# Performance work log

Hardware: AMD Instinct MI355X
Metric: run time of the kernel (lower is better)

## Reference

```python
import jax, jax.numpy as jnp
import numpy as np

WORD, D, H = 512, 64, 8  # word_size, embed_dim (per-head), n_query

def setup_inputs() -> dict:
    key = jax.random.key(0)
    ks = jax.random.split(key, 9)
    B, S = 2, 4096
    sw = 1.0 / np.sqrt(WORD)
    x  = jax.random.normal(ks[0], (B, S, WORD), dtype=jnp.float32)
    Wk = jax.random.normal(ks[1], (WORD, D), dtype=jnp.float32) * sw
    bk = jnp.zeros((D,), jnp.float32)
    Wv = jax.random.normal(ks[2], (WORD, D), dtype=jnp.float32) * sw
    bv = jnp.zeros((D,), jnp.float32)
    Wq = jax.random.normal(ks[3], (H, WORD, D), dtype=jnp.float32) * sw
    bq = jnp.zeros((H, D), jnp.float32)
    Wp = jax.random.normal(ks[4], (H * D, D), dtype=jnp.float32) * (1.0 / np.sqrt(H * D))
    bp = jnp.zeros((D,), jnp.float32)
    return {"x": x, "Wq": Wq, "bq": bq, "Wk": Wk, "bk": bk, "Wv": Wv, "bv": bv, "Wp": Wp, "bp": bp}

def reference(x, Wq, bq, Wk, bk, Wv, bv, Wp, bp):
    # shared K/V across all query heads (multi-query attention)
    K = x @ Wk + bk                                   # [b, s, d]
    V = x @ Wv + bv                                   # [b, s, d]
    Q = jnp.einsum('bsw,hwd->bhsd', x, Wq) + bq[None, :, None, :]  # [b, h, s, d]
    scale = 1.0 / jnp.sqrt(jnp.float32(D))
    scores = jnp.einsum('bhsd,btd->bhst', Q, K) * scale  # [b, h, s, t]
    attn = jax.nn.softmax(scores, axis=-1)
    Z = jnp.einsum('bhst,btd->bhsd', attn, V)            # [b, h, s, d]
    B, _, S, _ = Z.shape
    Zc = jnp.transpose(Z, (0, 2, 1, 3)).reshape(B, S, H * D)  # concat heads
    return Zc @ Wp + bp                                   # [b, s, d]
```

## Files before the change

kernel.cpp:

```cpp
#include <hip/hip_runtime.h>
#include <hip/hip_bf16.h>
#include <stdint.h>

#define BB 2
#define SS 4096
#define WW 512
#define DD 64
#define HH 8
#define QSCALE 0.1803368801111244f

typedef __hip_bfloat16 bf16;
typedef __bf16 bf16x8 __attribute__((ext_vector_type(8)));
typedef float f32x16 __attribute__((ext_vector_type(16)));
typedef unsigned int u32x4 __attribute__((ext_vector_type(4)));
typedef unsigned int u32x2 __attribute__((ext_vector_type(2)));

union U4 { u32x4 u4; unsigned int u[4]; bf16x8 v; };

__device__ __forceinline__ float ldv(const float* p, size_t i) { return p[i]; }
__device__ __forceinline__ float ldv(const bf16* p, size_t i)  { return __bfloat162float(p[i]); }

__device__ __forceinline__ unsigned short f2bu(float f) {
    union Ub { bf16 b; unsigned short u; } t;
    t.b = __float2bfloat16(f);
    return t.u;
}

__device__ __forceinline__ float fast_exp2(float x) {
#if __has_builtin(__builtin_amdgcn_exp2f)
    return __builtin_amdgcn_exp2f(x);
#else
    return exp2f(x);
#endif
}

__device__ __forceinline__ f32x16 mfma_bf16(bf16x8 a, bf16x8 b, f32x16 c) {
    return __builtin_amdgcn_mfma_f32_32x32x16_bf16(a, b, c, 0, 0, 0);
}

__device__ __forceinline__ unsigned int pk_bf16(float lo, float hi) {
    unsigned int a = __float_as_uint(lo) + 0x8000u;
    unsigned int b = __float_as_uint(hi) + 0x8000u;
    return __builtin_amdgcn_perm(b, a, 0x07060302u);
}

__device__ __forceinline__ int block_detect(const void* raw, int* cntLds)
{
    if (threadIdx.x == 0) *cntLds = 0;
    __syncthreads();
    const bf16* xb = (const bf16*)raw;
    const float v = __bfloat162float(xb[2 * threadIdx.x]);
    const float a = fabsf(v);
    const bool insane = !(v == v) || (a >= 1.0e4f) || (a != 0.0f && a <= 1.0e-8f);
    const unsigned long long m = __ballot(insane);
    if ((threadIdx.x & 63) == 0) atomicAdd(cntLds, __popcll(m));
    __syncthreads();
    return (*cntLds * 2 > 256) ? 1 : 0;
}

template<typename T> struct StReg;
template<> struct StReg<bf16>  { u32x4 v; };
template<> struct StReg<float> { float4 a, b; };

__device__ __forceinline__ void stld(StReg<bf16>& r, const bf16* p, size_t i) {
    r.v = *(const u32x4*)((const unsigned short*)p + i);
}
__device__ __forceinline__ void stld(StReg<float>& r, const float* p, size_t i) {
    r.a = *(const float4*)(p + i);
    r.b = *(const float4*)(p + i + 4);
}
__device__ __forceinline__ u32x4 stpack(const StReg<bf16>& r) { return r.v; }
__device__ __forceinline__ u32x4 stpack(const StReg<float>& r) {
    u32x4 w;
    w[0] = pk_bf16(r.a.x, r.a.y); w[1] = pk_bf16(r.a.z, r.a.w);
    w[2] = pk_bf16(r.b.x, r.b.y); w[3] = pk_bf16(r.b.z, r.b.w);
    return w;
}

template<typename T>
__device__ __forceinline__ void prep_w_body(
    const T* Wq, const T* bq, const T* Wk, const T* bk,
    const T* Wv, const T* bv, const T* Wp, const T* bp,
    unsigned short* Wb, float* bb, float (*Tt)[65], int pwblk)
{
    const int tid = threadIdx.x;
    const int cg = pwblk >> 3, wg = pwblk & 7;
    const int c0 = cg * 64, w0 = wg * 64;
    const T* src = (cg == 0) ? Wk : (cg == 1) ? Wv
                 : (cg == 10) ? Wp : (Wq + (size_t)(cg - 2) * WW * DD);
    const float scale = (cg >= 2 && cg < 10) ? QSCALE : 1.0f;

    #pragma unroll
    for (int i = 0; i < 16; ++i) {
        const int e = i * 256 + tid, w = e >> 6, d = e & 63;
        Tt[w][d] = ldv(src, (size_t)(w0 + w) * DD + d) * scale;
    }
    __syncthreads();
    #pragma unroll
    for (int i = 0; i < 16; ++i) {
        const int e = i * 256 + tid, d = e >> 6, w = e & 63;
        Wb[(size_t)(c0 + d) * WW + w0 + w] = f2bu(Tt[w][d]);
    }
    if (pwblk == 0) {
        #pragma unroll
        for (int i = 0; i < 3; ++i) {
            const int c = tid + i * 256;
            if (c < 704) {
                float v;
                if (c < 64)       v = ldv(bk, c);
                else if (c < 128) v = ldv(bv, c - 64);
                else if (c < 640) v = ldv(bq, c - 128) * QSCALE;
                else              v = ldv(bp, c - 640);
                bb[c] = v;
            }
        }
    }
}

__global__ __launch_bounds__(256) void wprep_kernel(
    const void* x, const void* Wq, const void* bq, const void* Wk, const void* bk,
    const void* Wv, const void* bv, const void* Wp, const void* bp,
    unsigned short* Wb, float* bb, int* flag)
{
    __shared__ float Tt[64][65];
    __shared__ int cnt;
    if (blockIdx.x == 0) {
        const int flx = block_detect(x, &cnt);
        if (threadIdx.x == 0) *flag = flx;
    }
    const int fl = block_detect(Wk, &cnt);
    if (fl)
        prep_w_body<float>((const float*)Wq, (const float*)bq, (const float*)Wk,
                           (const float*)bk, (const float*)Wv, (const float*)bv,
                           (const float*)Wp, (const float*)bp, Wb, bb, Tt, blockIdx.x);
    else
        prep_w_body<bf16>((const bf16*)Wq, (const bf16*)bq, (const bf16*)Wk,
                          (const bf16*)bk, (const bf16*)Wv, (const bf16*)bv,
                          (const bf16*)Wp, (const bf16*)bp, Wb, bb, Tt, blockIdx.x);
}

#define KP 40

template<typename T>
__device__ __forceinline__ void proj_body(
    const T* xsrc, const unsigned short* Wb, const float* bb,
    bf16* Kb, bf16* Qb, unsigned short* Vtg,
    unsigned short* As0, unsigned short* Bs0)
{
    const int tid = threadIdx.x;
    const int wv = tid >> 6, ln = tid & 63;
    const int g = ln >> 5, cc = ln & 31;
    const int nblk = blockIdx.x % 5, mblk = blockIdx.x / 5;
    const int row0 = mblk * 128, n0 = nblk * 128;
    const int wm = (wv & 1) * 64, wn = (wv >> 1) * 64;

    const int sm = tid >> 2;
    const int sko = (tid & 3) * 8;

    StReg<T> pa[2];
    u32x4 pb[2];
    #define GLOAD(kt)                                                          \
        do {                                                                   \
            _Pragma("unroll")                                                  \
            for (int i = 0; i < 2; ++i) {                                      \
                const int m = sm + i * 64;                                     \
                stld(pa[i], xsrc, (size_t)(row0 + m) * WW + (kt) * 32 + sko);  \
                pb[i] = *(const u32x4*)&Wb[(size_t)(n0 + m) * WW + (kt) * 32 + sko]; \
            }                                                                  \
        } while (0)
    #define LWRITE(buf)                                                        \
        do {                                                                   \
            _Pragma("unroll")                                                  \
            for (int i = 0; i < 2; ++i) {                                      \
                const int m = sm + i * 64;                                     \
                *(u32x4*)&As0[(buf) * (128 * KP) + m * KP + sko] = stpack(pa[i]); \
                *(u32x4*)&Bs0[(buf) * (128 * KP) + m * KP + sko] = pb[i];      \
            }                                                                  \
        } while (0)

    f32x16 acc[2][2];
    #pragma unroll
    for (int a = 0; a < 2; ++a)
        #pragma unroll
        for (int c2 = 0; c2 < 2; ++c2)
            #pragma unroll
            for (int i = 0; i < 16; ++i) acc[a][c2][i] = 0.f;

    GLOAD(0); LWRITE(0);
    GLOAD(1);

    for (int kt = 0; kt < 16; ++kt) {
        __syncthreads();
        const int buf = kt & 1;
        #pragma unroll
        for (int ks = 0; ks < 2; ++ks) {
            U4 af[2], bfr[2];
            #pragma unroll
            for (int ms = 0; ms < 2; ++ms)
                af[ms].u4 = *(const u32x4*)&As0[buf * (128 * KP) +
                                                (wm + ms * 32 + cc) * KP + ks * 16 + g * 8];
            #pragma unroll
            for (int ns = 0; ns < 2; ++ns)
                bfr[ns].u4 = *(const u32x4*)&Bs0[buf * (128 * KP) +
                                                 (wn + ns * 32 + cc) * KP + ks * 16 + g * 8];
            #pragma unroll
            for (int ms = 0; ms < 2; ++ms)
                #pragma unroll
                for (int ns = 0; ns < 2; ++ns)
                    acc[ms][ns] = mfma_bf16(af[ms].v, bfr[ns].v, acc[ms][ns]);
        }
        if (kt < 15) {
            LWRITE(buf ^ 1);
            if (kt < 14) GLOAD(kt + 2);
        }
    }
    #undef GLOAD
    #undef LWRITE

    const int b = row0 >> 12;
    #pragma unroll
    for (int ns = 0; ns < 2; ++ns) {
        const int c = n0 + wn + ns * 32 + cc;
        const int grp = c >> 6, d = c & 63;
        const float bias = bb[c];
        if (grp != 1) {
            bf16* base = (grp == 0) ? Kb
                       : Qb + (size_t)((b * HH + grp - 2) - b) * SS * DD;
            #pragma unroll
            for (int ms = 0; ms < 2; ++ms) {
                #pragma unroll
                for (int reg = 0; reg < 16; ++reg) {
                    const int r = (reg & 3) + 8 * (reg >> 2) + 4 * g;
                    const int row = row0 + wm + ms * 32 + r;
                    base[(size_t)row * DD + d] = __float2bfloat16(acc[ms][ns][reg] + bias);
                }
            }
        }
    }

    __syncthreads();
    unsigned short (*Vl)[65] = (unsigned short (*)[65])As0;
    if (nblk == 0 && wv >= 2) {
        #pragma unroll
        for (int ns = 0; ns < 2; ++ns) {
            const int d = ns * 32 + cc;
            const float bias = bb[64 + d];
            #pragma unroll
            for (int ms = 0; ms < 2; ++ms)
                #pragma unroll
                for (int reg = 0; reg < 16; ++reg) {
                    const int r = wm + ms * 32 + (reg & 3) + 8 * (reg >> 2) + 4 * g;
                    Vl[r][d] = f2bu(acc[ms][ns][reg] + bias);
                }
        }
    }
    __syncthreads();
    if (nblk == 0) {
        const int t0 = row0 & 4095;
        const int d = tid >> 2, tch = tid & 3;
        unsigned short* op = Vtg + ((size_t)b * DD + d) * SS + t0 + tch * 32;
        unsigned short tmp[32];
        #pragma unroll
        for (int j = 0; j < 32; ++j) tmp[j] = Vl[tch * 32 + j][d];
        const int soff[8] = {0, 8, 4, 12, 16, 24, 20, 28};
        #pragma unroll
        for (int jg = 0; jg < 8; ++jg) {
            u32x2 w2;
            w2[0] = (unsigned int)tmp[jg * 4 + 0] | ((unsigned int)tmp[jg * 4 + 1] << 16);
            w2[1] = (unsigned int)tmp[jg * 4 + 2] | ((unsigned int)tmp[jg * 4 + 3] << 16);
            *(u32x2*)&op[soff[jg]] = w2;
        }
    }
}

__global__ __launch_bounds__(256, 2) void proj_mfma_kernel(
    const void* x, const unsigned short* __restrict__ Wb,
    const float* __restrict__ bb,
    bf16* __restrict__ Kb, bf16* __restrict__ Qb, unsigned short* __restrict__ Vtg)
{
    __shared__ unsigned short As[2][128 * KP];
    __shared__ unsigned short Bs[2][128 * KP];
    __shared__ int cnt;
    const int fl = block_detect(x, &cnt);
    if (fl)
        proj_body<float>((const float*)x, Wb, bb, Kb, Qb, Vtg, &As[0][0], &Bs[0][0]);
    else
        proj_body<bf16>((const bf16*)x, Wb, bb, Kb, Qb, Vtg, &As[0][0], &Bs[0][0]);
}

#define VTP 72
#define ZP_PART ((size_t)16 * 64 * 4096)
#define LP_PART ((size_t)16 * 4096)

template<int TSPLIT>
__global__ __launch_bounds__(256, 4) void attn_mfma_kernel(
    const bf16* __restrict__ Kb, const unsigned short* __restrict__ Vtg,
    const bf16* __restrict__ Qb, bf16* __restrict__ Zb,
    float* __restrict__ Zp, float* __restrict__ Lp)
{
    __shared__ unsigned short Vt[2][64 * VTP];
    __shared__ unsigned short Kt[2][64 * VTP];

    const int tid = threadIdx.x;
    const int wv = tid >> 6, ln = tid & 63;
    const int g  = ln >> 5, cc = ln & 31;
    const int chunk = blockIdx.x & 31;
    const int tsp = (TSPLIT == 1) ? 0 : ((blockIdx.x / 32) % TSPLIT);
    const int bh  = blockIdx.x / (32 * TSPLIT);
    const int b = bh >> 3, h = bh & 7;
    const int qw = chunk * 128 + wv * 32;
    const int it0 = tsp * (64 / TSPLIT);
    const int itN = it0 + 64 / TSPLIT;

    const unsigned short* Kg = (const unsigned short*)(Kb + (size_t)b * SS * DD);
    const unsigned short* Vg = Vtg + (size_t)b * DD * SS;
    const char* Qg = (const char*)(Qb + (size_t)(b * HH + h) * SS * DD);

    const int sr = tid >> 2, sc = (tid & 3) * 16;
    const unsigned short* VgRow = Vg + (size_t)sr * SS;

    U4 qf[4];
    #pragma unroll
    for (int ks = 0; ks < 4; ++ks)
        qf[ks].u4 = *(const u32x4*)(Qg +
            (size_t)((qw + cc) * 64 + g * 8 + ks * 16) * 2);

    f32x16 zacc[2];
    #pragma unroll
    for (int dt = 0; dt < 2; ++dt)
        #pragma unroll
        for (int i = 0; i < 16; ++i) zacc[dt][i] = 0.f;

    float la = 0.f, lb2 = 0.f;

    {
        const unsigned short* ksrc = Kg + (size_t)(it0 * 64 + sr) * 64 + sc;
        const unsigned short* vsrc = VgRow + it0 * 64 + sc;
        *(u32x4*)&Kt[0][sr * VTP + sc + 0] = *(const u32x4*)&ksrc[0];
        *(u32x4*)&Kt[0][sr * VTP + sc + 8] = *(const u32x4*)&ksrc[8];
        *(u32x4*)&Vt[0][sr * VTP + sc + 0] = *(const u32x4*)&vsrc[0];
        *(u32x4*)&Vt[0][sr * VTP + sc + 8] = *(const u32x4*)&vsrc[8];
    }

    for (int it = it0; it < itN; ++it) {
        __syncthreads();
        const int buf = it & 1;
        const bool more = (it + 1) < itN;
        u32x4 pk0, pk1, pv0, pv1;
        if (more) {
            const unsigned short* ksrc = Kg + (size_t)((it + 1) * 64 + sr) * 64 + sc;
            const unsigned short* vsrc = VgRow + (it + 1) * 64 + sc;
            pk0 = *(const u32x4*)&ksrc[0];
            pk1 = *(const u32x4*)&ksrc[8];
            pv0 = *(const u32x4*)&vsrc[0];
            pv1 = *(const u32x4*)&vsrc[8];
        }

        #pragma unroll
        for (int si = 0; si < 2; ++si) {
            U4 kf[4];
            #pragma unroll
            for (int ks = 0; ks < 4; ++ks)
                kf[ks].u4 = *(const u32x4*)&Kt[buf][(si * 32 + cc) * VTP +
                                                    ks * 16 + g * 8];

            f32x16 s;
            #pragma unroll
            for (int i = 0; i < 16; ++i) s[i] = 0.f;
            #pragma unroll
            for (int ks = 0; ks < 4; ++ks) s = mfma_bf16(kf[ks].v, qf[ks].v, s);

            float p[16];
            #pragma unroll
            for (int i = 0; i < 16; ++i) p[i] = fast_exp2(s[i]);
            #pragma unroll
            for (int i = 0; i < 8; ++i) { la += p[i]; lb2 += p[8 + i]; }

            unsigned int w0[8];
            #pragma unroll
            for (int i2 = 0; i2 < 8; ++i2)
                w0[i2] = pk_bf16(p[2 * i2], p[2 * i2 + 1]);

            #pragma unroll
            for (int ks = 0; ks < 2; ++ks) {
                U4 pb;
                pb.u[0] = w0[ks * 4 + 0]; pb.u[1] = w0[ks * 4 + 1];
                pb.u[2] = w0[ks * 4 + 2]; pb.u[3] = w0[ks * 4 + 3];
                #pragma unroll
                for (int dt = 0; dt < 2; ++dt) {
                    U4 vf;
                    vf.u4 = *(const u32x4*)&Vt[buf][(dt * 32 + cc) * VTP +
                                                    si * 32 + ks * 16 + g * 8];
                    zacc[dt] = mfma_bf16(vf.v, pb.v, zacc[dt]);
                }
            }
        }

        if (more) {
            *(u32x4*)&Kt[buf ^ 1][sr * VTP + sc + 0] = pk0;
            *(u32x4*)&Kt[buf ^ 1][sr * VTP + sc + 8] = pk1;
            *(u32x4*)&Vt[buf ^ 1][sr * VTP + sc + 0] = pv0;
            *(u32x4*)&Vt[buf ^ 1][sr * VTP + sc + 8] = pv1;
        }
    }

    float l = la + lb2;
    l += __shfl_xor(l, 32, 64);

    if (TSPLIT == 1) {
        const float rr = 1.0f / l;
        bf16* zp = Zb + (size_t)(b * SS + qw + cc) * (HH * DD) + h * DD + g * 4;
        #pragma unroll
        for (int dt = 0; dt < 2; ++dt)
            #pragma unroll
            for (int i = 0; i < 16; ++i) {
                const int d = (i & 3) + 8 * (i >> 2) + 32 * dt;
                zp[d] = __float2bfloat16(zacc[dt][i] * rr);
            }
    } else {
        float* zp0 = Zp + (size_t)(tsp * 16 + bh) * (64 * 4096);
        #pragma unroll
        for (int dt = 0; dt < 2; ++dt)
            #pragma unroll
            for (int i = 0; i < 16; ++i) {
                const int d = (i & 3) + 8 * (i >> 2) + 4 * g + 32 * dt;
                zp0[(size_t)d * 4096 + qw + cc] = zacc[dt][i];
            }
        if (g == 0)
            Lp[(size_t)(tsp * 16 + bh) * 4096 + qw + cc] = l;
    }
}

template<int PARTS>
__global__ __launch_bounds__(256) void combine_kernel(
    const float* __restrict__ Zp, const float* __restrict__ Lp,
    bf16* __restrict__ Zb)
{
    const size_t T = (size_t)blockIdx.x * 256 + threadIdx.x;
    const int sblk = (int)(T & 511);
    const int d  = (int)((T >> 9) & 63);
    const int bh = (int)(T >> 15);
    const int s0 = sblk * 8;
    const int b = bh >> 3, h = bh & 7;

    float z[8], lv[8];
    #pragma unroll
    for (int j = 0; j < 8; ++j) { z[j] = 0.f; lv[j] = 0.f; }

    #pragma unroll
    for (int pp = 0; pp < PARTS; ++pp) {
        const float* p0 = Zp + pp * ZP_PART + ((size_t)bh * 64 + d) * 4096 + s0;
        const float* l0 = Lp + pp * LP_PART + (size_t)bh * 4096 + s0;
        #pragma unroll
        for (int j = 0; j < 8; j += 4) {
            const float4 a = *(const float4*)(p0 + j);
            z[j] += a.x; z[j+1] += a.y; z[j+2] += a.z; z[j+3] += a.w;
            const float4 e = *(const float4*)(l0 + j);
            lv[j] += e.x; lv[j+1] += e.y; lv[j+2] += e.z; lv[j+3] += e.w;
        }
    }
    bf16* zo = Zb + ((size_t)(b * SS + s0)) * (HH * DD) + h * DD + d;
    #pragma unroll
    for (int j = 0; j < 8; ++j)
        zo[(size_t)j * (HH * DD)] = __float2bfloat16(z[j] / lv[j]);
}

__global__ __launch_bounds__(256) void outp_mfma_kernel(
    const bf16* __restrict__ Zb, const unsigned short* __restrict__ Wb,
    const float* __restrict__ bb, const int* flag, void* out)
{
    __shared__ unsigned short As[2][128 * KP];
    __shared__ unsigned short Bs[2][64 * KP];

    const int tid = threadIdx.x;
    const int wv = tid >> 6, ln = tid & 63;
    const int g = ln >> 5, cc = ln & 31;
    const int row0 = blockIdx.x * 128;
    const int sm = tid >> 2, sko = (tid & 3) * 8;

    const unsigned short* Zu = (const unsigned short*)Zb;
    const unsigned short* Wn = Wb + (size_t)640 * WW;
    const float* bbp = bb + 640;

    u32x4 pa[2], pbv;
    #define GLOAD2(kt)                                                         \
        do {                                                                   \
            _Pragma("unroll")                                                  \
            for (int i = 0; i < 2; ++i)                                        \
                pa[i] = *(const u32x4*)&Zu[(size_t)(row0 + sm + i * 64) * WW + (kt) * 32 + sko]; \
            pbv = *(const u32x4*)&Wn[(size_t)sm * WW + (kt) * 32 + sko];       \
        } while (0)
    #define LWRITE2(buf)                                                       \
        do {                                                                   \
            _Pragma("unroll")                                                  \
            for (int i = 0; i < 2; ++i)                                        \
                *(u32x4*)&As[buf][(sm + i * 64) * KP + sko] = pa[i];           \
            *(u32x4*)&Bs[buf][sm * KP + sko] = pbv;                            \
        } while (0)

    f32x16 acc[2];
    #pragma unroll
    for (int ns = 0; ns < 2; ++ns)
        #pragma unroll
        for (int i = 0; i < 16; ++i) acc[ns][i] = 0.f;

    GLOAD2(0); LWRITE2(0);
    GLOAD2(1);

    for (int kt = 0; kt < 16; ++kt) {
        __syncthreads();
        const int buf = kt & 1;
        #pragma unroll
        for (int ks = 0; ks < 2; ++ks) {
            U4 af;
            af.u4 = *(const u32x4*)&As[buf][(wv * 32 + cc) * KP + ks * 16 + g * 8];
            #pragma unroll
            for (int ns = 0; ns < 2; ++ns) {
                U4 bf2;
                bf2.u4 = *(const u32x4*)&Bs[buf][(ns * 32 + cc) * KP + ks * 16 + g * 8];
                acc[ns] = mfma_bf16(af.v, bf2.v, acc[ns]);
            }
        }
        if (kt < 15) {
            LWRITE2(buf ^ 1);
            if (kt < 14) GLOAD2(kt + 2);
        }
    }
    #undef GLOAD2
    #undef LWRITE2

    const int fl = *flag;
    #pragma unroll
    for (int ns = 0; ns < 2; ++ns) {
        const int c = ns * 32 + cc;
        const float bias = bbp[c];
        #pragma unroll
        for (int reg = 0; reg < 16; ++reg) {
            const int r = (reg & 3) + 8 * (reg >> 2) + 4 * g;
            const int row = row0 + wv * 32 + r;
            const float v = acc[ns][reg] + bias;
            if (fl) ((float*)out)[(size_t)row * DD + c] = v;
            else    ((bf16*)out)[(size_t)row * DD + c] = __float2bfloat16(v);
        }
    }
}

extern "C" void kernel_launch(void* const* d_in, const int* in_sizes, int n_in,
                              void* d_out, int out_size, void* d_ws, size_t ws_size,
                              hipStream_t stream)
{
    const void* x  = d_in[0];
    const void* Wq = d_in[1];
    const void* bq = d_in[2];
    const void* Wk = d_in[3];
    const void* bk = d_in[4];
    const void* Wv = d_in[5];
    const void* bv = d_in[6];
    const void* Wp = d_in[7];
    const void* bp = d_in[8];

    char* ws = (char*)d_ws;
    bf16* Kb = (bf16*)(ws);
    bf16* Qb = (bf16*)(ws + (2u << 20));
    bf16* Zb = (bf16*)(ws + (10u << 20));
    int* flag = (int*)(ws + (18u << 20));
    unsigned short* Wb = (unsigned short*)(ws + (18u << 20) + 64);
    float* bb = (float*)(ws + (18u << 20) + 64 + 704 * 512 * 2);
    unsigned short* Vtg = (unsigned short*)(ws + (19u << 20));
    float* Zp = (float*)(ws + (20u << 20));

    const size_t base = (size_t)(20u << 20);
    const size_t need4 = base + 4 * ZP_PART * 4 + 4 * LP_PART * 4;
    const size_t need2 = base + 2 * ZP_PART * 4 + 2 * LP_PART * 4;

    wprep_kernel<<<88, 256, 0, stream>>>(x, Wq, bq, Wk, bk, Wv, bv, Wp, bp, Wb, bb, flag);
    proj_mfma_kernel<<<320, 256, 0, stream>>>(x, Wb, bb, Kb, Qb, Vtg);

    if (ws_size >= need4) {
        float* Lp = (float*)(ws + base + 4 * ZP_PART * 4);
        attn_mfma_kernel<4><<<16 * 32 * 4, 256, 0, stream>>>(Kb, Vtg, Qb, Zb, Zp, Lp);
        combine_kernel<4><<<2048, 256, 0, stream>>>(Zp, Lp, Zb);
    } else if (ws_size >= need2) {
        float* Lp = (float*)(ws + base + 2 * ZP_PART * 4);
        attn_mfma_kernel<2><<<16 * 32 * 2, 256, 0, stream>>>(Kb, Vtg, Qb, Zb, Zp, Lp);
        combine_kernel<2><<<2048, 256, 0, stream>>>(Zp, Lp, Zb);
    } else {
        float* Lp = (float*)(ws + base);
        attn_mfma_kernel<1><<<16 * 32, 256, 0, stream>>>(Kb, Vtg, Qb, Zb, Zp, Lp);
    }
    outp_mfma_kernel<<<64, 256, 0, stream>>>(Zb, Wb, bb, flag, d_out);
}
```

Before: 213.4 us.

## Software-pipeline softmax exp behind next QK MFMA and drop 4-way key split

Restructures the attention inner loop so the exp/pack/PV step for one 32-key subtile runs after the QK MFMA of the next subtile. The exp work can then overlap with matrix-core latency, and one pending score tile is carried across iterations. To keep the deferred V reads safe, a second barrier is added before the next tile is written to shared memory. The launcher also drops the 4-way key split and prefers the 2-way split, which means fewer partial sums to combine but fewer blocks in flight.

```diff
diff --git a/kernel.cpp b/kernel.cpp
--- a/kernel.cpp
+++ b/kernel.cpp
@@ -341,6 +341,37 @@
         *(u32x4*)&Vt[0][sr * VTP + sc + 0] = *(const u32x4*)&vsrc[0];
         *(u32x4*)&Vt[0][sr * VTP + sc + 8] = *(const u32x4*)&vsrc[8];
     }
+
+    f32x16 spend;
+    #pragma unroll
+    for (int i = 0; i < 16; ++i) spend[i] = -1.0e30f;
+    int pbuf = 0, ppos = 0;
+
+    #define RETIRE(sv, vb, vpos)                                               \
+        do {                                                                   \
+            float p[16];                                                       \
+            _Pragma("unroll")                                                  \
+            for (int i = 0; i < 16; ++i) p[i] = fast_exp2((sv)[i]);            \
+            _Pragma("unroll")                                                  \
+            for (int i = 0; i < 8; ++i) { la += p[i]; lb2 += p[8 + i]; }       \
+            unsigned int w0[8];                                                \
+            _Pragma("unroll")                                                  \
+            for (int i2 = 0; i2 < 8; ++i2)                                     \
+                w0[i2] = pk_bf16(p[2 * i2], p[2 * i2 + 1]);                    \
+            _Pragma("unroll")                                                  \
+            for (int ks = 0; ks < 2; ++ks) {                                   \
+                U4 pbf;                                                        \
+                pbf.u[0] = w0[ks * 4 + 0]; pbf.u[1] = w0[ks * 4 + 1];          \
+                pbf.u[2] = w0[ks * 4 + 2]; pbf.u[3] = w0[ks * 4 + 3];          \
+                _Pragma("unroll")                                              \
+                for (int dt = 0; dt < 2; ++dt) {                               \
+                    U4 vf;                                                     \
+                    vf.u4 = *(const u32x4*)&Vt[vb][(dt * 32 + cc) * VTP +      \
+                                                   (vpos) * 32 + ks * 16 + g * 8]; \
+                    zacc[dt] = mfma_bf16(vf.v, pbf.v, zacc[dt]);               \
+                }                                                              \
+            }                                                                  \
+        } while (0)
 
     for (int it = it0; it < itN; ++it) {
         __syncthreads();
@@ -356,53 +387,44 @@
             pv1 = *(const u32x4*)&vsrc[8];
         }
 
-        #pragma unroll
-        for (int si = 0; si < 2; ++si) {
+        f32x16 s0;
+        {
             U4 kf[4];
             #pragma unroll
             for (int ks = 0; ks < 4; ++ks)
-                kf[ks].u4 = *(const u32x4*)&Kt[buf][(si * 32 + cc) * VTP +
-                                                    ks * 16 + g * 8];
-
-            f32x16 s;
-            #pragma unroll
-            for (int i = 0; i < 16; ++i) s[i] = 0.f;
-            #pragma unroll
-            for (int ks = 0; ks < 4; ++ks) s = mfma_bf16(kf[ks].v, qf[ks].v, s);
-
-            float p[16];
-            #pragma unroll
-            for (int i = 0; i < 16; ++i) p[i] = fast_exp2(s[i]);
-            #pragma unroll
-            for (int i = 0; i < 8; ++i) { la += p[i]; lb2 += p[8 + i]; }
-
-            unsigned int w0[8];
-            #pragma unroll
-            for (int i2 = 0; i2 < 8; ++i2)
-                w0[i2] = pk_bf16(p[2 * i2], p[2 * i2 + 1]);
-
-            #pragma unroll
-            for (int ks = 0; ks < 2; ++ks) {
-                U4 pb;
-                pb.u[0] = w0[ks * 4 + 0]; pb.u[1] = w0[ks * 4 + 1];
-                pb.u[2] = w0[ks * 4 + 2]; pb.u[3] = w0[ks * 4 + 3];
-                #pragma unroll
-                for (int dt = 0; dt < 2; ++dt) {
-                    U4 vf;
-                    vf.u4 = *(const u32x4*)&Vt[buf][(dt * 32 + cc) * VTP +
-                                                    si * 32 + ks * 16 + g * 8];
-                    zacc[dt] = mfma_bf16(vf.v, pb.v, zacc[dt]);
-                }
-            }
-        }
+                kf[ks].u4 = *(const u32x4*)&Kt[buf][(cc) * VTP + ks * 16 + g * 8];
+            #pragma unroll
+            for (int i = 0; i < 16; ++i) s0[i] = 0.f;
+            #pragma unroll
+            for (int ks = 0; ks < 4; ++ks) s0 = mfma_bf16(kf[ks].v, qf[ks].v, s0);
+        }
+        RETIRE(spend, pbuf, ppos);
+
+        f32x16 s1;
+        {
+            U4 kf[4];
+            #pragma unroll
+            for (int ks = 0; ks < 4; ++ks)
+                kf[ks].u4 = *(const u32x4*)&Kt[buf][(32 + cc) * VTP + ks * 16 + g * 8];
+            #pragma unroll
+            for (int i = 0; i < 16; ++i) s1[i] = 0.f;
+            #pragma unroll
+            for (int ks = 0; ks < 4; ++ks) s1 = mfma_bf16(kf[ks].v, qf[ks].v, s1);
+        }
+        RETIRE(s0, buf, 0);
+
+        spend = s1; pbuf = buf; ppos = 1;
 
         if (more) {
+            __syncthreads();
             *(u32x4*)&Kt[buf ^ 1][sr * VTP + sc + 0] = pk0;
             *(u32x4*)&Kt[buf ^ 1][sr * VTP + sc + 8] = pk1;
             *(u32x4*)&Vt[buf ^ 1][sr * VTP + sc + 0] = pv0;
             *(u32x4*)&Vt[buf ^ 1][sr * VTP + sc + 8] = pv1;
         }
     }
+    RETIRE(spend, pbuf, ppos);
+    #undef RETIRE
 
     float l = la + lb2;
     l += __shfl_xor(l, 32, 64);
@@ -570,17 +592,12 @@
     float* Zp = (float*)(ws + (20u << 20));
 
     const size_t base = (size_t)(20u << 20);
-    const size_t need4 = base + 4 * ZP_PART * 4 + 4 * LP_PART * 4;
     const size_t need2 = base + 2 * ZP_PART * 4 + 2 * LP_PART * 4;
 
     wprep_kernel<<<88, 256, 0, stream>>>(x, Wq, bq, Wk, bk, Wv, bv, Wp, bp, Wb, bb, flag);
     proj_mfma_kernel<<<320, 256, 0, stream>>>(x, Wb, bb, Kb, Qb, Vtg);
 
-    if (ws_size >= need4) {
-        float* Lp = (float*)(ws + base + 4 * ZP_PART * 4);
-        attn_mfma_kernel<4><<<16 * 32 * 4, 256, 0, stream>>>(Kb, Vtg, Qb, Zb, Zp, Lp);
-        combine_kernel<4><<<2048, 256, 0, stream>>>(Zp, Lp, Zb);
-    } else if (ws_size >= need2) {
+    if (ws_size >= need2) {
         float* Lp = (float*)(ws + base + 2 * ZP_PART * 4);
         attn_mfma_kernel<2><<<16 * 32 * 2, 256, 0, stream>>>(Kb, Vtg, Qb, Zb, Zp, Lp);
         combine_kernel<2><<<2048, 256, 0, stream>>>(Zp, Lp, Zb);
```

New measurement: 250.4 us. +17.4%, slower.
